# Performance work log

Measured on AMD Instinct MI355X. Metric: run time of the kernel, lower is better.

## Reference

```python
import jax, jax.numpy as jnp
import numpy as np

B, L, D, H, E, K = 8, 2048, 512, 512, 256, 30


def setup_inputs() -> dict:
    key = jax.random.key(0)
    ks = jax.random.split(key, 10)
    init = lambda k, shape: (jax.random.normal(k, shape, jnp.float32) * 0.02)
    x = jax.random.normal(ks[0], (B, L, D), jnp.float32)
    # lengths in [L//2, L]; first one forced to L so max(x_lengths) == L (matches torch mask shape)
    rest = jax.random.randint(ks[9], (B - 1,), L // 2, L + 1).astype(jnp.int32)
    x_lengths = jnp.concatenate([jnp.array([L], jnp.int32), rest])
    return {
        "x": x,
        "w_g_w": init(ks[1], (D, H)), "w_g_b": init(ks[2], (H,)),
        "t1_w": init(ks[3], (D, E)), "t1_b": init(ks[4], (E,)),
        "t2_w": init(ks[5], (D, E)), "t2_b": init(ks[6], (E,)),
        "w_z_w": init(ks[7], (H, D)), "w_z_b": init(ks[8], (D,)),
        "x_lengths": x_lengths,
    }


def reference(x, w_g_w, w_g_b, t1_w, t1_b, t2_w, t2_b, w_z_w, w_z_b, x_lengths):
    # x: [B, L, D]
    x_prime = x @ w_g_w + w_g_b                      # [B, L, H]
    x1 = x @ t1_w + t1_b                             # [B, L, E]
    x2 = x @ t2_w + t2_b                             # [B, L, E]
    inter = jnp.einsum("bie,bje->bij", x1, x2)      # [B, L, L]
    att = jax.nn.softmax(inter, axis=-1)             # embedded_gaussian
    # key-side length mask (masks.permute([0,2,1]) in torch -> [B,1,L])
    mask = (jnp.arange(L)[None, :] < x_lengths[:, None]).astype(att.dtype)
    att = att * mask[:, None, :]
    att = att / jnp.sum(att, axis=-1, keepdims=True)
    # top-k clipping + scatter back into a zero matrix, then renormalize
    topk, idx = jax.lax.top_k(att, K)                # [B, L, K]
    bi = jnp.arange(B)[:, None, None]
    ri = jnp.arange(L)[None, :, None]
    att = jnp.zeros_like(att).at[bi, ri, idx].set(topk)
    att = att / jnp.sum(att, axis=-1, keepdims=True)
    y = att @ x_prime                                # [B, L, H]
    y = y @ w_z_w + w_z_b                            # [B, L, D]
    return x + y
```

## Files before the change

### kernel.cpp

```cpp
#include <hip/hip_runtime.h>


typedef _Float16 h2   __attribute__((ext_vector_type(2)));
typedef _Float16 h4   __attribute__((ext_vector_type(4)));
typedef _Float16 h8   __attribute__((ext_vector_type(8)));
typedef float    f32x4 __attribute__((ext_vector_type(4)));

__device__ __forceinline__ h2 as_h2(float f) {
    union { float f; h2 h; } u; u.f = f; return u.h;
}
__device__ __forceinline__ float packh2(float a, float b) {
    union { h2 h; float f; } u; u.h.x = (_Float16)a; u.h.y = (_Float16)b; return u.f;
}

__global__ __launch_bounds__(256) void k0_pack(
    const float* __restrict__ wg, const float* __restrict__ w1,
    const float* __restrict__ w2, const float* __restrict__ wz,
    _Float16* __restrict__ wT, _Float16* __restrict__ wzT)
{
    __shared__ float tile[32][33];
    const int id = blockIdx.x;
    const float* src; _Float16* dst; int Nd, n0, k0;
    if (id < 256)      { src = wg; dst = wT;            Nd = 512; n0 = (id & 15) * 32;        k0 = (id >> 4) * 32; }
    else if (id < 384) { src = w1; dst = wT + 512*512;  Nd = 256; n0 = ((id-256) & 7) * 32;   k0 = ((id-256) >> 3) * 32; }
    else if (id < 512) { src = w2; dst = wT + 768*512;  Nd = 256; n0 = ((id-384) & 7) * 32;   k0 = ((id-384) >> 3) * 32; }
    else               { src = wz; dst = wzT;           Nd = 512; n0 = ((id-512) & 15) * 32;  k0 = ((id-512) >> 4) * 32; }

    const int t = threadIdx.x;
    const int r = t >> 3, c = (t & 7) * 4;
    *(float4*)&tile[r][c] = *(const float4*)(src + (size_t)(k0 + r) * Nd + n0 + c);
    __syncthreads();
    h4 hv;
    hv.x = (_Float16)tile[c + 0][r];
    hv.y = (_Float16)tile[c + 1][r];
    hv.z = (_Float16)tile[c + 2][r];
    hv.w = (_Float16)tile[c + 3][r];
    *(h4*)(dst + (size_t)(n0 + r) * 512 + k0 + c) = hv;
}

__global__ __launch_bounds__(256) void k1_mfma(
    const float* __restrict__ x, const _Float16* __restrict__ wT,
    const float* __restrict__ bg, const float* __restrict__ b1,
    const float* __restrict__ b2,
    float* __restrict__ xph, float* __restrict__ x1p, float4* __restrict__ x2tn4)
{
    __shared__ __align__(16) char lds_raw[40960];
    _Float16* Alds = (_Float16*)lds_raw;
    _Float16* Blds = (_Float16*)(lds_raw + 8192);

    const int t = threadIdx.x;
    const int m0 = blockIdx.x * 64;
    const int cb = blockIdx.y;
    const int n0 = cb * 256;
    const int lane = t & 63, w = t >> 6;
    const int arow = lane & 15, ak = (lane >> 4) * 8;

    f32x4 acc[4][4];
    #pragma unroll
    for (int i = 0; i < 4; ++i)
        #pragma unroll
        for (int j = 0; j < 4; ++j) acc[i][j] = (f32x4){0.f, 0.f, 0.f, 0.f};

    for (int k0 = 0; k0 < 512; k0 += 64) {
        __syncthreads();
        {
            const int r = t >> 2, c0 = (t & 3) * 16;
            const float* src = x + (size_t)(m0 + r) * 512 + k0 + c0;
            #pragma unroll
            for (int hvi = 0; hvi < 2; ++hvi) {
                float4 u0 = *(const float4*)(src + hvi * 8);
                float4 u1 = *(const float4*)(src + hvi * 8 + 4);
                h8 hv;
                hv[0] = (_Float16)u0.x; hv[1] = (_Float16)u0.y;
                hv[2] = (_Float16)u0.z; hv[3] = (_Float16)u0.w;
                hv[4] = (_Float16)u1.x; hv[5] = (_Float16)u1.y;
                hv[6] = (_Float16)u1.z; hv[7] = (_Float16)u1.w;
                *(h8*)(Alds + r * 64 + c0 + hvi * 8) = hv;
            }
        }
        {
            #pragma unroll
            for (int i = 0; i < 8; ++i) {
                int idx = t + i * 256;
                int row = idx >> 3, ch = idx & 7;
                *(float4*)(Blds + row * 64 + ch * 8) =
                    *(const float4*)(wT + (size_t)(n0 + row) * 512 + k0 + ch * 8);
            }
        }
        __syncthreads();

        #pragma unroll
        for (int kk = 0; kk < 2; ++kk) {
            h8 af[4], bf[4];
            #pragma unroll
            for (int rb = 0; rb < 4; ++rb)
                af[rb] = *(const h8*)(Alds + (rb * 16 + arow) * 64 + kk * 32 + ak);
            #pragma unroll
            for (int cf = 0; cf < 4; ++cf)
                bf[cf] = *(const h8*)(Blds + (w * 64 + cf * 16 + arow) * 64 + kk * 32 + ak);
            #pragma unroll
            for (int rb = 0; rb < 4; ++rb)
                #pragma unroll
                for (int cf = 0; cf < 4; ++cf)
                    acc[rb][cf] = __builtin_amdgcn_mfma_f32_16x16x32_f16(
                        af[rb], bf[cf], acc[rb][cf], 0, 0, 0);
        }
    }

    const float* bias = (cb < 2) ? (bg + cb * 256) : (cb == 2 ? b1 : b2);

    if (cb < 3) {
        float* dst; int epbase; size_t rstr;
        if (cb < 2) { dst = xph; epbase = cb * 128; rstr = 256; }
        else        { dst = x1p; epbase = 0;        rstr = 128; }
        #pragma unroll
        for (int cf = 0; cf < 4; ++cf) {
            const int c = w * 64 + cf * 16 + arow;
            const float bv = bias[c];
            #pragma unroll
            for (int rb = 0; rb < 4; ++rb) {
                #pragma unroll
                for (int j = 0; j < 4; ++j) {
                    float v = acc[rb][cf][j] + bv;
                    float o = __shfl_xor(v, 1);
                    if ((lane & 1) == 0) {
                        int row = m0 + rb * 16 + (lane >> 4) * 4 + j;
                        dst[(size_t)row * rstr + epbase + (c >> 1)] = packh2(v, o);
                    }
                }
            }
        }
    } else {
        __syncthreads();
        float* T = (float*)lds_raw;
        #pragma unroll
        for (int cf = 0; cf < 4; ++cf) {
            const int c = w * 64 + cf * 16 + arow;
            const float bv = bias[c];
            #pragma unroll
            for (int rb = 0; rb < 4; ++rb) {
                #pragma unroll
                for (int j = 0; j < 4; ++j) {
                    float v = acc[rb][cf][j] + bv;
                    float o = __shfl_xor(v, 1);
                    if ((lane & 1) == 0)
                        T[(c >> 1) * 68 + rb * 16 + (lane >> 4) * 4 + j] = packh2(v, o);
                }
            }
        }
        __syncthreads();
        const int bb = m0 >> 11, j0 = m0 & 2047;
        #pragma unroll
        for (int g = 0; g < 8; ++g) {
            int slot = t + g * 256;
            int jt = slot >> 9;
            int ks = (slot >> 6) & 7;
            int l  = slot & 63;
            int eg = l >> 4, jc = l & 15;
            const float* Tp = T + (ks * 16 + eg * 4) * 68 + jt * 16 + jc;
            float4 v;
            v.x = Tp[0]; v.y = Tp[68]; v.z = Tp[136]; v.w = Tp[204];
            x2tn4[(((size_t)bb * 128 + (j0 >> 4) + jt) * 8 + ks) * 64 + l] = v;
        }
    }
}

__global__ __launch_bounds__(512, 4) void k2_attn(
    const float* __restrict__ x1p, const float4* __restrict__ x2tn4,
    const float* __restrict__ xph, const int* __restrict__ xlen,
    float* __restrict__ yah)
{
    __shared__ unsigned scU[16][1024];
    __shared__ unsigned cand[16][64];
    __shared__ unsigned tkp[16][30];
    __shared__ float    wvs[16][30];
    __shared__ int      tki[16][30];
    __shared__ float    vin[16];
    __shared__ unsigned rowmax[16];
    __shared__ int      cntA[16][2];
    __shared__ int      cntF[16];

    const int t  = threadIdx.x;
    const int b  = blockIdx.x & 7;
    const int i0 = (blockIdx.x >> 3) * 16;
    const int hfirst = (blockIdx.x >> 3) & 1;
    const int len = xlen[b];
    const int lane = t & 63, wid = t >> 6;

    ((unsigned*)cand)[t] = 0u;
    ((unsigned*)cand)[t + 512] = 0u;
    if (t < 32) cntA[t >> 1][t & 1] = 0;
    if (t < 16) cntF[t] = 0;

    h8 afr[8];
    {
        const int ar = lane & 15;
        const float* x1row = x1p + ((size_t)b * 2048 + i0 + ar) * 128 + (lane >> 4) * 4;
        #pragma unroll
        for (int ks = 0; ks < 8; ++ks)
            afr[ks] = *(const h8*)(x1row + ks * 16);
    }

    const float4* x2b = x2tn4 + ((size_t)b * 128) * 8 * 64 + lane;
    const int jcol  = lane & 15;
    const int rbase = (lane >> 4) * 4;

#define LOADT(H, NT, DST)                                                   \
    {                                                                       \
        const float4* pb_ = x2b + (size_t)(((H) * 64 + wid * 8 + (NT)) * 8) * 64; \
        _Pragma("unroll")                                                   \
        for (int ks = 0; ks < 8; ++ks)                                      \
            DST[ks] = *(const h8*)(pb_ + ks * 64);                          \
    }

#define MFMAT(H, NT, SRC)                                                   \
    {                                                                       \
        const int j_ = (H) * 1024 + wid * 128 + (NT) * 16 + jcol;           \
        const int cs_ = wid * 128 + (NT) * 16 + jcol;                       \
        f32x4 acc = (f32x4){0.f, 0.f, 0.f, 0.f};                            \
        _Pragma("unroll")                                                   \
        for (int ks = 0; ks < 8; ++ks)                                      \
            acc = __builtin_amdgcn_mfma_f32_16x16x32_f16(afr[ks], SRC[ks], acc, 0, 0, 0); \
        const unsigned tag = (unsigned)(2047 - j_);                         \
        const bool valid = (j_ < len);                                      \
        _Pragma("unroll")                                                   \
        for (int jj = 0; jj < 4; ++jj) {                                    \
            unsigned bb = __float_as_uint(acc[jj]);                         \
            bb = bb ^ (0x80000000u | (unsigned)((int)bb >> 31));            \
            scU[rbase + jj][cs_] = valid ? ((bb & 0xFFFFF800u) | tag) : 0u; \
        }                                                                   \
    }

    for (int hh = 0; hh < 2; ++hh) {
        const int h = hfirst ^ hh;
        {
            h8 va[8], vb[8];
            LOADT(h, 0, va)
            LOADT(h, 1, vb)
            MFMAT(h, 0, va)  LOADT(h, 2, va)
            MFMAT(h, 1, vb)  LOADT(h, 3, vb)
            MFMAT(h, 2, va)  LOADT(h, 4, va)
            MFMAT(h, 3, vb)  LOADT(h, 5, vb)
            MFMAT(h, 4, va)  LOADT(h, 6, va)
            MFMAT(h, 5, vb)  LOADT(h, 7, vb)
            MFMAT(h, 6, va)
            MFMAT(h, 7, vb)
        }
        __syncthreads();

        #pragma unroll
        for (int rr = 0; rr < 2; ++rr) {
            const int row = wid * 2 + rr;
            unsigned u0[16];
            #pragma unroll
            for (int c = 0; c < 4; ++c)
                *(uint4*)&u0[c * 4] = *(const uint4*)&scU[row][lane * 4 + c * 256];

            unsigned P = 0u;
            for (int bit = 31; bit >= 0; --bit) {
                const unsigned cd = P | (1u << bit);
                int cnt = 0;
                #pragma unroll
                for (int q = 0; q < 16; ++q)
                    cnt += (int)__popcll(__ballot(u0[q] >= cd));
                if (cnt >= 30) {
                    P = cd;
                    if (cnt == 30) break;
                }
            }
            #pragma unroll
            for (int q = 0; q < 16; ++q) {
                if (u0[q] >= P && u0[q] != 0u) {
                    int s = atomicAdd(&cntA[row][h], 1);
                    cand[row][h * 30 + s] = u0[q];
                }
            }
        }
        __syncthreads();
    }
#undef LOADT
#undef MFMAT

    #pragma unroll
    for (int rr = 0; rr < 2; ++rr) {
        const int row = wid * 2 + rr;
        unsigned v = (lane < 60) ? cand[row][lane] : 0u;
        unsigned lm = v;
        #pragma unroll
        for (int off = 32; off > 0; off >>= 1) {
            unsigned o = (unsigned)__shfl_xor((int)lm, off);
            lm = lm > o ? lm : o;
        }
        if (lane == 0) rowmax[row] = lm;

        unsigned P = 0u;
        for (int bit = 31; bit >= 0; --bit) {
            const unsigned cd = P | (1u << bit);
            int cnt = (int)__popcll(__ballot(v >= cd));
            if (cnt >= 30) {
                P = cd;
                if (cnt == 30) break;
            }
        }
        if (v >= P && v != 0u) {
            int s = atomicAdd(&cntF[row], 1);
            tkp[row][s] = v;
        }
    }
    __syncthreads();

    {
        const int r = t >> 5, k = t & 31;
        if (k < 30) {
            unsigned u = tkp[r][k];
            unsigned m0 = rowmax[r] & 0xFFFFF800u;
            unsigned ub = u & 0xFFFFF800u;
            unsigned bb0 = (m0 & 0x80000000u) ? (m0 ^ 0x80000000u) : ~m0;
            unsigned bbk = (ub & 0x80000000u) ? (ub ^ 0x80000000u) : ~ub;
            float s0 = __uint_as_float(bb0);
            float sk = __uint_as_float(bbk);
            wvs[r][k] = __expf(sk - s0);
            tki[r][k] = 2047 - (int)(u & 0x7FFu);
        }
    }
    __syncthreads();
    if (t < 16) {
        float s = 0.f;
        #pragma unroll
        for (int k = 0; k < 30; ++k) s += wvs[t][k];
        vin[t] = 1.f / s;
    }
    __syncthreads();

    const int g  = t >> 8;
    const int hp = t & 255;
    for (int r = g * 8; r < g * 8 + 8; ++r) {
        float y0 = 0.f, y1 = 0.f;
        #pragma unroll
        for (int k = 0; k < 30; ++k) {
            int j = tki[r][k];
            float wv = wvs[r][k];
            h2 u = as_h2(xph[((size_t)b * 2048 + j) * 256 + hp]);
            y0 = fmaf(wv, (float)u.x, y0);
            y1 = fmaf(wv, (float)u.y, y1);
        }
        const float inv = vin[r];
        yah[((size_t)b * 2048 + i0 + r) * 256 + hp] = packh2(y0 * inv, y1 * inv);
    }
}

__global__ __launch_bounds__(256) void k3_mfma(
    const float* __restrict__ yah, const _Float16* __restrict__ wzT,
    const float* __restrict__ bz, const float* __restrict__ x,
    float* __restrict__ out)
{
    __shared__ __align__(16) char lds_raw[40960];
    _Float16* Alds = (_Float16*)lds_raw;
    _Float16* Blds = (_Float16*)(lds_raw + 8192);

    const int t = threadIdx.x;
    const int m0 = blockIdx.x * 64;
    const int n0 = blockIdx.y * 256;
    const int lane = t & 63, w = t >> 6;
    const int arow = lane & 15, ak = (lane >> 4) * 8;

    f32x4 acc[4][4];
    #pragma unroll
    for (int i = 0; i < 4; ++i)
        #pragma unroll
        for (int j = 0; j < 4; ++j) acc[i][j] = (f32x4){0.f, 0.f, 0.f, 0.f};

    for (int k0 = 0; k0 < 512; k0 += 64) {
        __syncthreads();
        {
            const int r = t >> 2, c0 = (t & 3) * 8;
            const float4* src = (const float4*)(yah + (size_t)(m0 + r) * 256 + k0 / 2 + c0);
            float4* dst = (float4*)(Alds + r * 64 + c0 * 2);
            dst[0] = src[0]; dst[1] = src[1];
        }
        {
            #pragma unroll
            for (int i = 0; i < 8; ++i) {
                int idx = t + i * 256;
                int row = idx >> 3, ch = idx & 7;
                *(float4*)(Blds + row * 64 + ch * 8) =
                    *(const float4*)(wzT + (size_t)(n0 + row) * 512 + k0 + ch * 8);
            }
        }
        __syncthreads();

        #pragma unroll
        for (int kk = 0; kk < 2; ++kk) {
            h8 af[4], bf[4];
            #pragma unroll
            for (int rb = 0; rb < 4; ++rb)
                af[rb] = *(const h8*)(Alds + (rb * 16 + arow) * 64 + kk * 32 + ak);
            #pragma unroll
            for (int cf = 0; cf < 4; ++cf)
                bf[cf] = *(const h8*)(Blds + (w * 64 + cf * 16 + arow) * 64 + kk * 32 + ak);
            #pragma unroll
            for (int rb = 0; rb < 4; ++rb)
                #pragma unroll
                for (int cf = 0; cf < 4; ++cf)
                    acc[rb][cf] = __builtin_amdgcn_mfma_f32_16x16x32_f16(
                        af[rb], bf[cf], acc[rb][cf], 0, 0, 0);
        }
    }

    #pragma unroll
    for (int cf = 0; cf < 4; ++cf) {
        const int c = n0 + w * 64 + cf * 16 + arow;
        const float bv = bz[c];
        #pragma unroll
        for (int rb = 0; rb < 4; ++rb) {
            #pragma unroll
            for (int j = 0; j < 4; ++j) {
                int row = m0 + rb * 16 + (lane >> 4) * 4 + j;
                out[(size_t)row * 512 + c] =
                    acc[rb][cf][j] + bv + x[(size_t)row * 512 + c];
            }
        }
    }
}

extern "C" void kernel_launch(void* const* d_in, const int* in_sizes, int n_in,
                              void* d_out, int out_size, void* d_ws, size_t ws_size,
                              hipStream_t stream)
{
    (void)in_sizes; (void)n_in; (void)out_size; (void)ws_size;

    const float* x   = (const float*)d_in[0];
    const float* wg  = (const float*)d_in[1];
    const float* bg  = (const float*)d_in[2];
    const float* w1  = (const float*)d_in[3];
    const float* b1  = (const float*)d_in[4];
    const float* w2  = (const float*)d_in[5];
    const float* b2  = (const float*)d_in[6];
    const float* wzw = (const float*)d_in[7];
    const float* wzb = (const float*)d_in[8];
    const int* xlen  = (const int*)d_in[9];
    float* outp      = (float*)d_out;

    char* ws = (char*)d_ws;
    _Float16* wT   = (_Float16*)(ws);
    _Float16* wzT  = (_Float16*)(ws + 1u * 1024 * 1024);
    float* x1pw    = (float*)(ws +  2u * 1024 * 1024);
    float4* x2tnw  = (float4*)(ws + 10u * 1024 * 1024);
    float* xphw    = (float*)(ws + 18u * 1024 * 1024);
    float* yahw    = (float*)(ws + 34u * 1024 * 1024);

    hipLaunchKernelGGL(k0_pack, dim3(768), dim3(256), 0, stream,
                       wg, w1, w2, wzw, wT, wzT);
    hipLaunchKernelGGL(k1_mfma, dim3(256, 4), dim3(256), 0, stream,
                       x, wT, bg, b1, b2, xphw, x1pw, x2tnw);
    hipLaunchKernelGGL(k2_attn, dim3(1024), dim3(512), 0, stream,
                       x1pw, x2tnw, xphw, xlen, yahw);
    hipLaunchKernelGGL(k3_mfma, dim3(256, 2), dim3(256), 0, stream,
                       yahw, wzT, wzb, x, outp);
}
```

Baseline: 203.8 us.

## Split attention score pass into four quarters to halve LDS and raise occupancy

```diff
diff --git a/kernel.cpp b/kernel.cpp
--- a/kernel.cpp
+++ b/kernel.cpp
@@ -165,31 +165,32 @@
     }
 }
 
-__global__ __launch_bounds__(512, 4) void k2_attn(
+__global__ __launch_bounds__(512, 6) void k2_attn(
     const float* __restrict__ x1p, const float4* __restrict__ x2tn4,
     const float* __restrict__ xph, const int* __restrict__ xlen,
     float* __restrict__ yah)
 {
-    __shared__ unsigned scU[16][1024];
-    __shared__ unsigned cand[16][64];
+    __shared__ unsigned scU[16][512];
+    __shared__ unsigned cand[16][128];
     __shared__ unsigned tkp[16][30];
     __shared__ float    wvs[16][30];
     __shared__ int      tki[16][30];
     __shared__ float    vin[16];
     __shared__ unsigned rowmax[16];
-    __shared__ int      cntA[16][2];
+    __shared__ int      cntA[16][4];
     __shared__ int      cntF[16];
 
     const int t  = threadIdx.x;
     const int b  = blockIdx.x & 7;
     const int i0 = (blockIdx.x >> 3) * 16;
-    const int hfirst = (blockIdx.x >> 3) & 1;
+    const int qfirst = (blockIdx.x >> 3) & 3;
     const int len = xlen[b];
     const int lane = t & 63, wid = t >> 6;
 
-    ((unsigned*)cand)[t] = 0u;
-    ((unsigned*)cand)[t + 512] = 0u;
-    if (t < 32) cntA[t >> 1][t & 1] = 0;
+    #pragma unroll
+    for (int i = 0; i < 4; ++i)
+        ((unsigned*)cand)[t + i * 512] = 0u;
+    if (t < 64) cntA[t >> 2][t & 3] = 0;
     if (t < 16) cntF[t] = 0;
 
     h8 afr[8];
@@ -205,18 +206,18 @@
     const int jcol  = lane & 15;
     const int rbase = (lane >> 4) * 4;
 
-#define LOADT(H, NT, DST)                                                   \
+#define LOADT(Q, NT, DST)                                                   \
     {                                                                       \
-        const float4* pb_ = x2b + (size_t)(((H) * 64 + wid * 8 + (NT)) * 8) * 64; \
+        const float4* pb_ = x2b + (size_t)(((Q) * 32 + wid * 4 + (NT)) * 8) * 64; \
         _Pragma("unroll")                                                   \
         for (int ks = 0; ks < 8; ++ks)                                      \
             DST[ks] = *(const h8*)(pb_ + ks * 64);                          \
     }
 
-#define MFMAT(H, NT, SRC)                                                   \
+#define MFMAT(Q, NT, SRC)                                                   \
     {                                                                       \
-        const int j_ = (H) * 1024 + wid * 128 + (NT) * 16 + jcol;           \
-        const int cs_ = wid * 128 + (NT) * 16 + jcol;                       \
+        const int j_ = (Q) * 512 + wid * 64 + (NT) * 16 + jcol;             \
+        const int cs_ = wid * 64 + (NT) * 16 + jcol;                        \
         f32x4 acc = (f32x4){0.f, 0.f, 0.f, 0.f};                            \
         _Pragma("unroll")                                                   \
         for (int ks = 0; ks < 8; ++ks)                                      \
@@ -231,29 +232,25 @@
         }                                                                   \
     }
 
-    for (int hh = 0; hh < 2; ++hh) {
-        const int h = hfirst ^ hh;
+    for (int qq = 0; qq < 4; ++qq) {
+        const int q = (qfirst + qq) & 3;
         {
             h8 va[8], vb[8];
-            LOADT(h, 0, va)
-            LOADT(h, 1, vb)
-            MFMAT(h, 0, va)  LOADT(h, 2, va)
-            MFMAT(h, 1, vb)  LOADT(h, 3, vb)
-            MFMAT(h, 2, va)  LOADT(h, 4, va)
-            MFMAT(h, 3, vb)  LOADT(h, 5, vb)
-            MFMAT(h, 4, va)  LOADT(h, 6, va)
-            MFMAT(h, 5, vb)  LOADT(h, 7, vb)
-            MFMAT(h, 6, va)
-            MFMAT(h, 7, vb)
+            LOADT(q, 0, va)
+            LOADT(q, 1, vb)
+            MFMAT(q, 0, va)  LOADT(q, 2, va)
+            MFMAT(q, 1, vb)  LOADT(q, 3, vb)
+            MFMAT(q, 2, va)
+            MFMAT(q, 3, vb)
         }
         __syncthreads();
 
         #pragma unroll
         for (int rr = 0; rr < 2; ++rr) {
             const int row = wid * 2 + rr;
-            unsigned u0[16];
-            #pragma unroll
-            for (int c = 0; c < 4; ++c)
+            unsigned u0[8];
+            #pragma unroll
+            for (int c = 0; c < 2; ++c)
                 *(uint4*)&u0[c * 4] = *(const uint4*)&scU[row][lane * 4 + c * 256];
 
             unsigned P = 0u;
@@ -261,18 +258,18 @@
                 const unsigned cd = P | (1u << bit);
                 int cnt = 0;
                 #pragma unroll
-                for (int q = 0; q < 16; ++q)
-                    cnt += (int)__popcll(__ballot(u0[q] >= cd));
+                for (int qv = 0; qv < 8; ++qv)
+                    cnt += (int)__popcll(__ballot(u0[qv] >= cd));
                 if (cnt >= 30) {
                     P = cd;
                     if (cnt == 30) break;
                 }
             }
             #pragma unroll
-            for (int q = 0; q < 16; ++q) {
-                if (u0[q] >= P && u0[q] != 0u) {
-                    int s = atomicAdd(&cntA[row][h], 1);
-                    cand[row][h * 30 + s] = u0[q];
+            for (int qv = 0; qv < 8; ++qv) {
+                if (u0[qv] >= P && u0[qv] != 0u) {
+                    int s = atomicAdd(&cntA[row][q], 1);
+                    cand[row][q * 30 + s] = u0[qv];
                 }
             }
         }
@@ -284,8 +281,9 @@
     #pragma unroll
     for (int rr = 0; rr < 2; ++rr) {
         const int row = wid * 2 + rr;
-        unsigned v = (lane < 60) ? cand[row][lane] : 0u;
-        unsigned lm = v;
+        unsigned v0 = (lane < 120) ? cand[row][lane] : 0u;
+        unsigned v1 = (lane + 64 < 120) ? cand[row][lane + 64] : 0u;
+        unsigned lm = v0 > v1 ? v0 : v1;
         #pragma unroll
         for (int off = 32; off > 0; off >>= 1) {
             unsigned o = (unsigned)__shfl_xor((int)lm, off);
@@ -296,16 +294,15 @@
         unsigned P = 0u;
         for (int bit = 31; bit >= 0; --bit) {
             const unsigned cd = P | (1u << bit);
-            int cnt = (int)__popcll(__ballot(v >= cd));
+            int cnt = (int)__popcll(__ballot(v0 >= cd))
+                    + (int)__popcll(__ballot(v1 >= cd));
             if (cnt >= 30) {
                 P = cd;
                 if (cnt == 30) break;
             }
         }
-        if (v >= P && v != 0u) {
-            int s = atomicAdd(&cntF[row], 1);
-            tkp[row][s] = v;
-        }
+        if (v0 >= P && v0 != 0u) { int s = atomicAdd(&cntF[row], 1); tkp[row][s] = v0; }
+        if (v1 >= P && v1 != 0u) { int s = atomicAdd(&cntF[row], 1); tkp[row][s] = v1; }
     }
     __syncthreads();
 
```

Result: slower. 228.4 us (+12.0%).
